# Kernel optimization log

Hardware: AMD Instinct MI355X
Metric: run time of the kernel (lower is better)

## Reference

```python
import jax, jax.numpy as jnp
import numpy as np


def setup_inputs() -> dict:
    key = jax.random.key(0)
    ks = jax.random.split(key, 7)
    G, MC, B = 4, 100, 512
    IN, H, OUT = 456, 400, 10
    return {
        "x": jax.random.normal(ks[0], (B, IN), dtype=jnp.float32),
        "mu1": jax.random.normal(ks[1], (G, IN, H), dtype=jnp.float32),
        "sigma1": jax.random.normal(ks[2], (G, IN, H), dtype=jnp.float32),
        "mu3": jax.random.normal(ks[3], (G, H, OUT), dtype=jnp.float32),
        "sigma3": jax.random.normal(ks[4], (G, H, OUT), dtype=jnp.float32),
        "zeta1": jax.random.normal(ks[5], (G, MC, B, H), dtype=jnp.float32),
        "zeta3": jax.random.normal(ks[6], (G, MC, B, OUT), dtype=jnp.float32),
        "num": 3,
    }


def reference(x, mu1, sigma1, mu3, sigma3, zeta1, zeta3, num):
    # softplus(sigma)^2, the local-reparameterization variance term
    sp2 = lambda s: jnp.square(jnp.log1p(jnp.exp(s)))

    def one_net(m1, s1, m3, s3, z1, z3):
        # layer 1: local reparameterization trick (Kingma et al. 2015)
        g1 = x @ m1                               # [B, H]
        d1 = (x * x) @ sp2(s1)                    # [B, H]
        h = jax.nn.relu(g1 + jnp.sqrt(d1) * z1)   # [MC, B, H] via broadcast
        # layer 2
        g3 = jnp.einsum('mbh,ho->mbo', h, m3)     # [MC, B, OUT]
        d3 = jnp.einsum('mbh,ho->mbo', h * h, sp2(s3))
        o = jax.nn.relu(g3 + jnp.sqrt(d3) * z3)
        p = jax.nn.softmax(o, axis=-1)            # nn.Softmax over class dim
        return p.mean(axis=0)                     # average over MC samples

    G = num + 1
    outs = jax.vmap(one_net)(mu1[:G], sigma1[:G], mu3[:G], sigma3[:G],
                             zeta1[:G], zeta3[:G])  # [G, B, OUT]
    B = x.shape[0]
    # torch.cat((out_0, out_1, ...), dim=1)
    return jnp.transpose(outs, (1, 0, 2)).reshape(B, -1)
```

## Files before the change

### kernel.cpp

```cpp
#include <hip/hip_runtime.h>
#include <math.h>

#define GN  4
#define MCN 100
#define BN  512
#define INN 456
#define HN  400
#define ON  10

__device__ __forceinline__ float sp2f(float s) {
    float l = log1pf(__expf(-fabsf(s)));
    float r = fmaxf(s, 0.0f) + l;
    return r * r;
}

__global__ __launch_bounds__(256) void k_zero(float* __restrict__ out) {
    int i = blockIdx.x * 256 + threadIdx.x;
    if (i < BN * GN * ON) out[i] = 0.0f;
}

__global__ __launch_bounds__(256) void k_transpose(
    const float* __restrict__ x, float* __restrict__ xT, float* __restrict__ xxT) {
    __shared__ float tile[64][65];
    int it = blockIdx.x;
    int bt = blockIdx.y;
    int tx = threadIdx.x & 63;
    int ty = threadIdx.x >> 6;
    int i_in = it * 64 + tx;
    #pragma unroll
    for (int r = 0; r < 16; ++r) {
        int row = r * 4 + ty;
        int b = bt * 64 + row;
        tile[row][tx] = (i_in < INN) ? x[b * INN + i_in] : 0.0f;
    }
    __syncthreads();
    #pragma unroll
    for (int r = 0; r < 16; ++r) {
        int row = r * 4 + ty;
        int i = it * 64 + row;
        if (i < INN) {
            float v = tile[tx][row];
            xT[i * BN + bt * 64 + tx]  = v;
            xxT[i * BN + bt * 64 + tx] = v * v;
        }
    }
}

__global__ __launch_bounds__(256) void k_sp1(
    const float* __restrict__ sigma1, float* __restrict__ sp1) {
    int idx = blockIdx.x * 256 + threadIdx.x;
    const int n4 = GN * INN * HN / 4;
    if (idx < n4) {
        float4 s = ((const float4*)sigma1)[idx];
        float4 o;
        o.x = sp2f(s.x); o.y = sp2f(s.y); o.z = sp2f(s.z); o.w = sp2f(s.w);
        ((float4*)sp1)[idx] = o;
    }
}

__global__ __launch_bounds__(256) void k_layer1(
    const float* __restrict__ xT, const float* __restrict__ xxT,
    const float* __restrict__ mu1, const float* __restrict__ sp1,
    float* __restrict__ A, float* __restrict__ S) {
    int bt = blockIdx.x;
    int ht = blockIdx.y;
    int g  = blockIdx.z;
    int lane = threadIdx.x & 63;
    int wv   = threadIdx.x >> 6;
    int h = ht * 64 + lane;
    bool hv = h < HN;
    int hc = hv ? h : (HN - 1);
    int b0 = __builtin_amdgcn_readfirstlane(bt * 16 + wv * 4);
    const float* mp = mu1 + (size_t)g * INN * HN + hc;
    const float* pp = sp1 + (size_t)g * INN * HN + hc;
    float accA[4] = {0.f, 0.f, 0.f, 0.f};
    float accD[4] = {0.f, 0.f, 0.f, 0.f};
    #pragma unroll 4
    for (int k = 0; k < INN; ++k) {
        float a = mp[(size_t)k * HN];
        float p = pp[(size_t)k * HN];
        float4 xv  = *(const float4*)(xT  + k * BN + b0);
        float4 xxv = *(const float4*)(xxT + k * BN + b0);
        accA[0] = fmaf(a, xv.x,  accA[0]);
        accA[1] = fmaf(a, xv.y,  accA[1]);
        accA[2] = fmaf(a, xv.z,  accA[2]);
        accA[3] = fmaf(a, xv.w,  accA[3]);
        accD[0] = fmaf(p, xxv.x, accD[0]);
        accD[1] = fmaf(p, xxv.y, accD[1]);
        accD[2] = fmaf(p, xxv.z, accD[2]);
        accD[3] = fmaf(p, xxv.w, accD[3]);
    }
    if (hv) {
        #pragma unroll
        for (int j = 0; j < 4; ++j) {
            size_t o = ((size_t)g * BN + (b0 + j)) * HN + h;
            A[o] = accA[j];
            S[o] = sqrtf(accD[j]);
        }
    }
}

__global__ __launch_bounds__(256, 3) void k_layer2(
    const float* __restrict__ A, const float* __restrict__ S,
    const float* __restrict__ mu3, const float* __restrict__ sigma3,
    const float* __restrict__ zeta1, const float* __restrict__ zeta3,
    float* __restrict__ out) {
    int b  = blockIdx.x;
    int g  = blockIdx.y;
    int mb = blockIdx.z * 64;

    __shared__ float as_s[2 * HN];
    __shared__ float wv_s[HN * 20];
    __shared__ float outsh[16][ON];

    int t = threadIdx.x;

    for (int i = t; i < HN; i += 256) {
        size_t src = ((size_t)g * BN + b) * HN + i;
        as_s[2 * i]     = A[src];
        as_s[2 * i + 1] = S[src];
    }
    for (int i = t; i < HN * ON; i += 256) {
        int h = i / ON, o = i % ON;
        int wslot = (o < 4) ? o       : (o < 8) ? (4 + o) : (8 + o);
        int vslot = (o < 4) ? (4 + o) : (o < 8) ? (8 + o) : (10 + o);
        size_t src = (size_t)(g * HN + h) * ON + o;
        wv_s[h * 20 + wslot] = mu3[src];
        wv_s[h * 20 + vslot] = sp2f(sigma3[src]);
    }
    __syncthreads();

    int rg = t >> 4;
    int kc = t & 15;

    float accg[4][ON], accd[4][ON];
    #pragma unroll
    for (int i = 0; i < 4; ++i)
        #pragma unroll
        for (int o = 0; o < ON; ++o) { accg[i][o] = 0.0f; accd[i][o] = 0.0f; }

    const float* zp[4];
    #pragma unroll
    for (int i = 0; i < 4; ++i) {
        int m = mb + rg + 16 * i;
        int mcl = m < MCN ? m : (MCN - 1);
        zp[i] = zeta1 + ((size_t)(g * MCN + mcl) * BN + b) * HN + kc;
    }

    float zc[4];
    #pragma unroll
    for (int i = 0; i < 4; ++i) zc[i] = zp[i][0];

    #pragma unroll 1
    for (int j = 0; j < 25; ++j) {
        float zn[4];
        if (j < 24) {
            #pragma unroll
            for (int i = 0; i < 4; ++i) zn[i] = zp[i][16 * (j + 1)];
        } else {
            #pragma unroll
            for (int i = 0; i < 4; ++i) zn[i] = 0.0f;
        }
        int k = kc + 16 * j;
        float2 as = *(const float2*)(as_s + 2 * k);
        const float* wr = wv_s + k * 20;
        float4 w03 = *(const float4*)(wr);
        float4 v03 = *(const float4*)(wr + 4);
        float4 w47 = *(const float4*)(wr + 8);
        float4 v47 = *(const float4*)(wr + 12);
        float4 t4  = *(const float4*)(wr + 16);
        #pragma unroll
        for (int i = 0; i < 4; ++i) {
            float hval = fmaxf(0.0f, fmaf(as.y, zc[i], as.x));
            float h2 = hval * hval;
            accg[i][0] = fmaf(hval, w03.x, accg[i][0]);
            accg[i][1] = fmaf(hval, w03.y, accg[i][1]);
            accg[i][2] = fmaf(hval, w03.z, accg[i][2]);
            accg[i][3] = fmaf(hval, w03.w, accg[i][3]);
            accg[i][4] = fmaf(hval, w47.x, accg[i][4]);
            accg[i][5] = fmaf(hval, w47.y, accg[i][5]);
            accg[i][6] = fmaf(hval, w47.z, accg[i][6]);
            accg[i][7] = fmaf(hval, w47.w, accg[i][7]);
            accg[i][8] = fmaf(hval, t4.x,  accg[i][8]);
            accg[i][9] = fmaf(hval, t4.y,  accg[i][9]);
            accd[i][0] = fmaf(h2, v03.x, accd[i][0]);
            accd[i][1] = fmaf(h2, v03.y, accd[i][1]);
            accd[i][2] = fmaf(h2, v03.z, accd[i][2]);
            accd[i][3] = fmaf(h2, v03.w, accd[i][3]);
            accd[i][4] = fmaf(h2, v47.x, accd[i][4]);
            accd[i][5] = fmaf(h2, v47.y, accd[i][5]);
            accd[i][6] = fmaf(h2, v47.z, accd[i][6]);
            accd[i][7] = fmaf(h2, v47.w, accd[i][7]);
            accd[i][8] = fmaf(h2, t4.z,  accd[i][8]);
            accd[i][9] = fmaf(h2, t4.w,  accd[i][9]);
        }
        #pragma unroll
        for (int i = 0; i < 4; ++i) zc[i] = zn[i];
    }

    #pragma unroll
    for (int i = 0; i < 4; ++i) {
        #pragma unroll
        for (int o = 0; o < ON; ++o) {
            float vg = accg[i][o], vd = accd[i][o];
            vg += __shfl_xor(vg, 1);  vd += __shfl_xor(vd, 1);
            vg += __shfl_xor(vg, 2);  vd += __shfl_xor(vd, 2);
            vg += __shfl_xor(vg, 4);  vd += __shfl_xor(vd, 4);
            vg += __shfl_xor(vg, 8);  vd += __shfl_xor(vd, 8);
            accg[i][o] = vg; accd[i][o] = vd;
        }
    }

    if (kc == 0) {
        float psum[ON];
        #pragma unroll
        for (int o = 0; o < ON; ++o) psum[o] = 0.0f;
        #pragma unroll
        for (int i = 0; i < 4; ++i) {
            int m = mb + rg + 16 * i;
            if (m < MCN) {
                const float* z3p = zeta3 + ((size_t)(g * MCN + m) * BN + b) * ON;
                float ov[ON];
                float mx = 0.0f;
                #pragma unroll
                for (int o = 0; o < ON; ++o) {
                    float v = fmaf(sqrtf(accd[i][o]), z3p[o], accg[i][o]);
                    v = fmaxf(v, 0.0f);
                    ov[o] = v;
                    mx = fmaxf(mx, v);
                }
                float se = 0.0f;
                #pragma unroll
                for (int o = 0; o < ON; ++o) { float e = __expf(ov[o] - mx); ov[o] = e; se += e; }
                float r = 1.0f / se;
                #pragma unroll
                for (int o = 0; o < ON; ++o) psum[o] = fmaf(ov[o], r, psum[o]);
            }
        }
        #pragma unroll
        for (int o = 0; o < ON; ++o) outsh[rg][o] = psum[o];
    }
    __syncthreads();
    if (t < ON) {
        float s = 0.0f;
        #pragma unroll
        for (int r = 0; r < 16; ++r) s += outsh[r][t];
        atomicAdd(&out[b * (GN * ON) + g * ON + t], s * (1.0f / MCN));
    }
}

extern "C" void kernel_launch(void* const* d_in, const int* in_sizes, int n_in,
                              void* d_out, int out_size, void* d_ws, size_t ws_size,
                              hipStream_t stream) {
    const float* x      = (const float*)d_in[0];
    const float* mu1    = (const float*)d_in[1];
    const float* sigma1 = (const float*)d_in[2];
    const float* mu3    = (const float*)d_in[3];
    const float* sigma3 = (const float*)d_in[4];
    const float* zeta1  = (const float*)d_in[5];
    const float* zeta3  = (const float*)d_in[6];

    float* ws  = (float*)d_ws;
    float* xT  = ws;
    float* xxT = xT  + INN * BN;
    float* sp1 = xxT + INN * BN;
    float* A   = sp1 + GN * INN * HN;
    float* S   = A   + GN * BN * HN;
    float* out = (float*)d_out;

    k_zero<<<dim3((BN * GN * ON + 255) / 256), 256, 0, stream>>>(out);
    k_transpose<<<dim3(8, 8), 256, 0, stream>>>(x, xT, xxT);
    k_sp1<<<dim3((GN * INN * HN / 4 + 255) / 256), 256, 0, stream>>>(sigma1, sp1);
    k_layer1<<<dim3(32, 7, GN), 256, 0, stream>>>(xT, xxT, mu1, sp1, A, S);
    k_layer2<<<dim3(BN, GN, 2), 256, 0, stream>>>(A, S, mu3, sigma3, zeta1, zeta3, out);
}
```

Before: 668.9 us.

## Split layer2 g/d accumulators across threads, loop MC chunks per block, drop atomics

Layer 2 now gives the mean and variance accumulations to different half-groups of threads, which halves the accumulator registers per thread and allows 4 blocks per CU. Each block now covers all 100 MC samples for one (b,g) in chunks of 32 with an LDS epilogue, so the zeroing kernel and the atomicAdd are gone. Softplus for sigma3 is precomputed in the combined sp kernel, and the 16-lane reductions use DPP instead of shuffles. In exchange, half the grid blocks, extra barriers per chunk, and each thread recomputing the relu value for its half.

Result: faster. 588.0 us (-12.1%).

```diff
diff --git a/kernel.cpp b/kernel.cpp
--- a/kernel.cpp
+++ b/kernel.cpp
@@ -14,9 +14,16 @@
     return r * r;
 }
 
-__global__ __launch_bounds__(256) void k_zero(float* __restrict__ out) {
-    int i = blockIdx.x * 256 + threadIdx.x;
-    if (i < BN * GN * ON) out[i] = 0.0f;
+#define DPP_ADD(v, CTRL) \
+    ((v) + __int_as_float(__builtin_amdgcn_update_dpp( \
+        0, __float_as_int(v), (CTRL), 0xF, 0xF, true)))
+
+__device__ __forceinline__ float reduce16(float v) {
+    v = DPP_ADD(v, 0xB1);
+    v = DPP_ADD(v, 0x4E);
+    v = DPP_ADD(v, 0x124);
+    v = DPP_ADD(v, 0x128);
+    return v;
 }
 
 __global__ __launch_bounds__(256) void k_transpose(
@@ -46,15 +53,23 @@
     }
 }
 
-__global__ __launch_bounds__(256) void k_sp1(
-    const float* __restrict__ sigma1, float* __restrict__ sp1) {
+__global__ __launch_bounds__(256) void k_sp(
+    const float* __restrict__ sigma1, const float* __restrict__ sigma3,
+    float* __restrict__ sp1, float* __restrict__ sp3) {
     int idx = blockIdx.x * 256 + threadIdx.x;
-    const int n4 = GN * INN * HN / 4;
-    if (idx < n4) {
+    const int n1 = GN * INN * HN / 4;
+    const int n3 = GN * HN * ON / 4;
+    if (idx < n1) {
         float4 s = ((const float4*)sigma1)[idx];
         float4 o;
         o.x = sp2f(s.x); o.y = sp2f(s.y); o.z = sp2f(s.z); o.w = sp2f(s.w);
         ((float4*)sp1)[idx] = o;
+    } else if (idx < n1 + n3) {
+        int k = idx - n1;
+        float4 s = ((const float4*)sigma3)[k];
+        float4 o;
+        o.x = sp2f(s.x); o.y = sp2f(s.y); o.z = sp2f(s.z); o.w = sp2f(s.w);
+        ((float4*)sp3)[k] = o;
     }
 }
 
@@ -100,152 +115,163 @@
     }
 }
 
-__global__ __launch_bounds__(256, 3) void k_layer2(
+template<int NI>
+__device__ __forceinline__ void mc_chunk(
+    int g, int b, int mb, int kc, int og, int rgg, int t,
+    const float* __restrict__ zeta1, const float* __restrict__ zeta3,
+    const float* as_s, const float* wp, float* epi, float* psum) {
+    float acc[NI][ON];
+    #pragma unroll
+    for (int i = 0; i < NI; ++i)
+        #pragma unroll
+        for (int o = 0; o < ON; ++o) acc[i][o] = 0.0f;
+
+    const float* zp[NI];
+    #pragma unroll
+    for (int i = 0; i < NI; ++i) {
+        int m = mb + rgg + 8 * i;
+        int mcl = m < MCN ? m : (MCN - 1);
+        zp[i] = zeta1 + ((size_t)(g * MCN + mcl) * BN + b) * HN + kc;
+    }
+
+    float zc[NI];
+    #pragma unroll
+    for (int i = 0; i < NI; ++i) zc[i] = zp[i][0];
+
+    #pragma unroll 1
+    for (int j = 0; j < 25; ++j) {
+        float zn[NI];
+        if (j < 24) {
+            #pragma unroll
+            for (int i = 0; i < NI; ++i) zn[i] = zp[i][16 * (j + 1)];
+        } else {
+            #pragma unroll
+            for (int i = 0; i < NI; ++i) zn[i] = 0.0f;
+        }
+        float2 as = *(const float2*)(as_s + 2 * (kc + 16 * j));
+        const float* wr = wp + j * 160;
+        float2 w01 = *(const float2*)(wr);
+        float2 w23 = *(const float2*)(wr + 2);
+        float2 w45 = *(const float2*)(wr + 4);
+        float2 w67 = *(const float2*)(wr + 6);
+        float2 w89 = *(const float2*)(wr + 8);
+        #pragma unroll
+        for (int i = 0; i < NI; ++i) {
+            float hv = fmaxf(0.0f, fmaf(as.y, zc[i], as.x));
+            float c = og ? hv * hv : hv;
+            acc[i][0] = fmaf(c, w01.x, acc[i][0]);
+            acc[i][1] = fmaf(c, w01.y, acc[i][1]);
+            acc[i][2] = fmaf(c, w23.x, acc[i][2]);
+            acc[i][3] = fmaf(c, w23.y, acc[i][3]);
+            acc[i][4] = fmaf(c, w45.x, acc[i][4]);
+            acc[i][5] = fmaf(c, w45.y, acc[i][5]);
+            acc[i][6] = fmaf(c, w67.x, acc[i][6]);
+            acc[i][7] = fmaf(c, w67.y, acc[i][7]);
+            acc[i][8] = fmaf(c, w89.x, acc[i][8]);
+            acc[i][9] = fmaf(c, w89.y, acc[i][9]);
+        }
+        #pragma unroll
+        for (int i = 0; i < NI; ++i) zc[i] = zn[i];
+    }
+
+    #pragma unroll
+    for (int i = 0; i < NI; ++i)
+        #pragma unroll
+        for (int o = 0; o < ON; ++o) acc[i][o] = reduce16(acc[i][o]);
+
+    if (kc == 0) {
+        #pragma unroll
+        for (int i = 0; i < NI; ++i) {
+            int rl = rgg + 8 * i;
+            #pragma unroll
+            for (int o = 0; o < ON; ++o)
+                epi[(rl * ON + o) * 2 + og] = acc[i][o];
+        }
+    }
+    __syncthreads();
+
+    const int NR = NI * 8;
+    if (t < NR) {
+        int m = mb + t;
+        if (m < MCN) {
+            const float* z3p = zeta3 + ((size_t)(g * MCN + m) * BN + b) * ON;
+            float ov[ON];
+            float mx = 0.0f;
+            #pragma unroll
+            for (int o = 0; o < ON; ++o) {
+                float2 gd = *(const float2*)(epi + (t * ON + o) * 2);
+                float v = fmaf(sqrtf(gd.y), z3p[o], gd.x);
+                v = fmaxf(v, 0.0f);
+                ov[o] = v;
+                mx = fmaxf(mx, v);
+            }
+            float se = 0.0f;
+            #pragma unroll
+            for (int o = 0; o < ON; ++o) { float e = __expf(ov[o] - mx); ov[o] = e; se += e; }
+            float r = 1.0f / se;
+            #pragma unroll
+            for (int o = 0; o < ON; ++o) psum[o] = fmaf(ov[o], r, psum[o]);
+        }
+    }
+    __syncthreads();
+}
+
+__global__ __launch_bounds__(256, 4) void k_layer2(
     const float* __restrict__ A, const float* __restrict__ S,
-    const float* __restrict__ mu3, const float* __restrict__ sigma3,
+    const float* __restrict__ mu3, const float* __restrict__ sp3,
     const float* __restrict__ zeta1, const float* __restrict__ zeta3,
     float* __restrict__ out) {
-    int b  = blockIdx.x;
-    int g  = blockIdx.y;
-    int mb = blockIdx.z * 64;
-
-    __shared__ float as_s[2 * HN];
-    __shared__ float wv_s[HN * 20];
-    __shared__ float outsh[16][ON];
+    int b = blockIdx.x;
+    int g = blockIdx.y;
+
+    __shared__ __align__(16) float w_s[HN * ON];
+    __shared__ __align__(16) float v_s[HN * ON];
+    __shared__ __align__(16) float as_s[2 * HN];
+    __shared__ __align__(16) float epi[32 * ON * 2];
+    __shared__ __align__(16) float psh[32 * ON];
 
     int t = threadIdx.x;
 
+    {
+        const float4* wsrc = (const float4*)(mu3 + (size_t)g * HN * ON);
+        const float4* vsrc = (const float4*)(sp3 + (size_t)g * HN * ON);
+        for (int i = t; i < HN * ON / 4; i += 256) {
+            ((float4*)w_s)[i] = wsrc[i];
+            ((float4*)v_s)[i] = vsrc[i];
+        }
+    }
     for (int i = t; i < HN; i += 256) {
         size_t src = ((size_t)g * BN + b) * HN + i;
         as_s[2 * i]     = A[src];
         as_s[2 * i + 1] = S[src];
     }
-    for (int i = t; i < HN * ON; i += 256) {
-        int h = i / ON, o = i % ON;
-        int wslot = (o < 4) ? o       : (o < 8) ? (4 + o) : (8 + o);
-        int vslot = (o < 4) ? (4 + o) : (o < 8) ? (8 + o) : (10 + o);
-        size_t src = (size_t)(g * HN + h) * ON + o;
-        wv_s[h * 20 + wslot] = mu3[src];
-        wv_s[h * 20 + vslot] = sp2f(sigma3[src]);
-    }
-    __syncthreads();
-
-    int rg = t >> 4;
-    int kc = t & 15;
-
-    float accg[4][ON], accd[4][ON];
-    #pragma unroll
-    for (int i = 0; i < 4; ++i)
-        #pragma unroll
-        for (int o = 0; o < ON; ++o) { accg[i][o] = 0.0f; accd[i][o] = 0.0f; }
-
-    const float* zp[4];
-    #pragma unroll
-    for (int i = 0; i < 4; ++i) {
-        int m = mb + rg + 16 * i;
-        int mcl = m < MCN ? m : (MCN - 1);
-        zp[i] = zeta1 + ((size_t)(g * MCN + mcl) * BN + b) * HN + kc;
-    }
-
-    float zc[4];
-    #pragma unroll
-    for (int i = 0; i < 4; ++i) zc[i] = zp[i][0];
+    __syncthreads();
+
+    int kc  = t & 15;
+    int og  = (t >> 4) & 1;
+    int rgg = t >> 5;
+
+    const float* wp = (og ? v_s : w_s) + kc * ON;
+
+    float psum[ON];
+    #pragma unroll
+    for (int o = 0; o < ON; ++o) psum[o] = 0.0f;
 
     #pragma unroll 1
-    for (int j = 0; j < 25; ++j) {
-        float zn[4];
-        if (j < 24) {
-            #pragma unroll
-            for (int i = 0; i < 4; ++i) zn[i] = zp[i][16 * (j + 1)];
-        } else {
-            #pragma unroll
-            for (int i = 0; i < 4; ++i) zn[i] = 0.0f;
-        }
-        int k = kc + 16 * j;
-        float2 as = *(const float2*)(as_s + 2 * k);
-        const float* wr = wv_s + k * 20;
-        float4 w03 = *(const float4*)(wr);
-        float4 v03 = *(const float4*)(wr + 4);
-        float4 w47 = *(const float4*)(wr + 8);
-        float4 v47 = *(const float4*)(wr + 12);
-        float4 t4  = *(const float4*)(wr + 16);
-        #pragma unroll
-        for (int i = 0; i < 4; ++i) {
-            float hval = fmaxf(0.0f, fmaf(as.y, zc[i], as.x));
-            float h2 = hval * hval;
-            accg[i][0] = fmaf(hval, w03.x, accg[i][0]);
-            accg[i][1] = fmaf(hval, w03.y, accg[i][1]);
-            accg[i][2] = fmaf(hval, w03.z, accg[i][2]);
-            accg[i][3] = fmaf(hval, w03.w, accg[i][3]);
-            accg[i][4] = fmaf(hval, w47.x, accg[i][4]);
-            accg[i][5] = fmaf(hval, w47.y, accg[i][5]);
-            accg[i][6] = fmaf(hval, w47.z, accg[i][6]);
-            accg[i][7] = fmaf(hval, w47.w, accg[i][7]);
-            accg[i][8] = fmaf(hval, t4.x,  accg[i][8]);
-            accg[i][9] = fmaf(hval, t4.y,  accg[i][9]);
-            accd[i][0] = fmaf(h2, v03.x, accd[i][0]);
-            accd[i][1] = fmaf(h2, v03.y, accd[i][1]);
-            accd[i][2] = fmaf(h2, v03.z, accd[i][2]);
-            accd[i][3] = fmaf(h2, v03.w, accd[i][3]);
-            accd[i][4] = fmaf(h2, v47.x, accd[i][4]);
-            accd[i][5] = fmaf(h2, v47.y, accd[i][5]);
-            accd[i][6] = fmaf(h2, v47.z, accd[i][6]);
-            accd[i][7] = fmaf(h2, v47.w, accd[i][7]);
-            accd[i][8] = fmaf(h2, t4.z,  accd[i][8]);
-            accd[i][9] = fmaf(h2, t4.w,  accd[i][9]);
-        }
-        #pragma unroll
-        for (int i = 0; i < 4; ++i) zc[i] = zn[i];
-    }
-
-    #pragma unroll
-    for (int i = 0; i < 4; ++i) {
-        #pragma unroll
-        for (int o = 0; o < ON; ++o) {
-            float vg = accg[i][o], vd = accd[i][o];
-            vg += __shfl_xor(vg, 1);  vd += __shfl_xor(vd, 1);
-            vg += __shfl_xor(vg, 2);  vd += __shfl_xor(vd, 2);
-            vg += __shfl_xor(vg, 4);  vd += __shfl_xor(vd, 4);
-            vg += __shfl_xor(vg, 8);  vd += __shfl_xor(vd, 8);
-            accg[i][o] = vg; accd[i][o] = vd;
-        }
-    }
-
-    if (kc == 0) {
-        float psum[ON];
-        #pragma unroll
-        for (int o = 0; o < ON; ++o) psum[o] = 0.0f;
-        #pragma unroll
-        for (int i = 0; i < 4; ++i) {
-            int m = mb + rg + 16 * i;
-            if (m < MCN) {
-                const float* z3p = zeta3 + ((size_t)(g * MCN + m) * BN + b) * ON;
-                float ov[ON];
-                float mx = 0.0f;
-                #pragma unroll
-                for (int o = 0; o < ON; ++o) {
-                    float v = fmaf(sqrtf(accd[i][o]), z3p[o], accg[i][o]);
-                    v = fmaxf(v, 0.0f);
-                    ov[o] = v;
-                    mx = fmaxf(mx, v);
-                }
-                float se = 0.0f;
-                #pragma unroll
-                for (int o = 0; o < ON; ++o) { float e = __expf(ov[o] - mx); ov[o] = e; se += e; }
-                float r = 1.0f / se;
-                #pragma unroll
-                for (int o = 0; o < ON; ++o) psum[o] = fmaf(ov[o], r, psum[o]);
-            }
-        }
-        #pragma unroll
-        for (int o = 0; o < ON; ++o) outsh[rg][o] = psum[o];
+    for (int c = 0; c < 3; ++c)
+        mc_chunk<4>(g, b, c * 32, kc, og, rgg, t, zeta1, zeta3, as_s, wp, epi, psum);
+    mc_chunk<1>(g, b, 96, kc, og, rgg, t, zeta1, zeta3, as_s, wp, epi, psum);
+
+    if (t < 32) {
+        #pragma unroll
+        for (int o = 0; o < ON; ++o) psh[t * ON + o] = psum[o];
     }
     __syncthreads();
     if (t < ON) {
         float s = 0.0f;
         #pragma unroll
-        for (int r = 0; r < 16; ++r) s += outsh[r][t];
-        atomicAdd(&out[b * (GN * ON) + g * ON + t], s * (1.0f / MCN));
+        for (int r = 0; r < 32; ++r) s += psh[r * ON + t];
+        out[b * (GN * ON) + g * ON + t] = s * (1.0f / MCN);
     }
 }
 
@@ -264,13 +290,14 @@
     float* xT  = ws;
     float* xxT = xT  + INN * BN;
     float* sp1 = xxT + INN * BN;
-    float* A   = sp1 + GN * INN * HN;
+    float* sp3 = sp1 + GN * INN * HN;
+    float* A   = sp3 + GN * HN * ON;
     float* S   = A   + GN * BN * HN;
     float* out = (float*)d_out;
 
-    k_zero<<<dim3((BN * GN * ON + 255) / 256), 256, 0, stream>>>(out);
+    const int nsp = GN * INN * HN / 4 + GN * HN * ON / 4;
     k_transpose<<<dim3(8, 8), 256, 0, stream>>>(x, xT, xxT);
-    k_sp1<<<dim3((GN * INN * HN / 4 + 255) / 256), 256, 0, stream>>>(sigma1, sp1);
+    k_sp<<<dim3((nsp + 255) / 256), 256, 0, stream>>>(sigma1, sigma3, sp1, sp3);
     k_layer1<<<dim3(32, 7, GN), 256, 0, stream>>>(xT, xxT, mu1, sp1, A, S);
-    k_layer2<<<dim3(BN, GN, 2), 256, 0, stream>>>(A, S, mu3, sigma3, zeta1, zeta3, out);
-}
+    k_layer2<<<dim3(BN, GN), 256, 0, stream>>>(A, S, mu3, sp3, zeta1, zeta3, out);
+}
```
